# Optimization experiments

Hardware: AMD Instinct MI355X
Metric: run time of the kernel (lower is better)

## Reference

```python
import jax, jax.numpy as jnp
import numpy as np

M, IN, OUT = 8192, 4096, 4096
BITWIDTH = 7


def psto_shift_int32(x, shift):
    """Pseudo-stochastic right-shift of int32 x by `shift` bits -> int8.
    Faithful to PstoShiftInt32: floor-divide, derive a pseudo random number
    from the low half of the remainder, compare against the high half."""
    pow_s = jnp.left_shift(jnp.int32(1), shift)
    rt = jnp.floor_divide(x, pow_s)
    prob = jnp.abs(x - rt * pow_s)
    half_pow = jnp.left_shift(jnp.int32(1), shift // 2)
    qp = jnp.floor_divide(prob, half_pow)
    prn = prob - qp * half_pow
    prn = jnp.where(shift % 2 == 1, prn * 2, prn)
    dec = jnp.where(qp <= prn, jnp.int32(0), jnp.int32(1)) * jnp.sign(x)
    return jnp.clip(rt + dec, -127, 127).astype(jnp.int8)


def range_bitwidth(x):
    # RangeEstimate: ceil(log2(max|x|)), 0 if all-zero (torch also goes via float)
    m = jnp.max(jnp.abs(x)).astype(jnp.float32)
    return jnp.where(m == 0, jnp.int32(0), jnp.ceil(jnp.log2(m)).astype(jnp.int32))


def act_calc(acc, exp_in):
    """Shift int32 accumulator back to int8 and track the block exponent."""
    bw = range_bitwidth(acc)
    shift = bw - BITWIDTH
    # shift>1 -> shift by `shift`; shift==1 -> shift by 2; else -> plain int8 cast
    eff = jnp.where(shift > 1, shift, jnp.where(shift == 1, jnp.int32(2), jnp.int32(0)))
    rounded = psto_shift_int32(acc, jnp.maximum(eff, 0))
    out = jnp.where(eff > 0, rounded, acc.astype(jnp.int8))  # int8 cast wraps, as in torch
    exp_out = (exp_in + eff).astype(jnp.int8)
    return out, exp_out


def setup_inputs() -> dict:
    key = jax.random.key(0)
    k1, k2 = jax.random.split(key)
    # int8-valued tensors kept in int32 containers for the matmul accumulate
    act_in = jax.random.randint(k1, (M, IN), -127, 128, dtype=jnp.int32)
    weight = jax.random.randint(k2, (OUT, IN), -127, 128, dtype=jnp.int32)
    return {"act_in": act_in, "exp_in": -6, "weight": weight, "weight_exp": -9}


def reference(act_in, exp_in, weight, weight_exp):
    # the roundoff4 padding in the original is a no-op)
    acc = jnp.matmul(act_in, weight.T)  # [M, OUT] int32
    act_out, exp_out = act_calc(acc, jnp.int32(exp_in) + jnp.int32(weight_exp))
    return act_out, exp_out
```

## Files before the change

kernel.cpp:

```cpp
#include <hip/hip_runtime.h>
#include <stdint.h>
#include <math.h>

#define M_DIM 8192
#define N_DIM 4096
#define K_DIM 4096
#define BITWIDTH 7

#define BM 256
#define BN 128
#define BK 128
#define NT (K_DIM / BK)

using i32x4  = __attribute__((ext_vector_type(4)))  int;
using i32x16 = __attribute__((ext_vector_type(16))) int;

#define FENCE asm volatile("" ::: "memory")

__global__ __launch_bounds__(256) void pack_both_kernel(
        const int* __restrict__ act, const int* __restrict__ wt,
        uint32_t* __restrict__ a8p, uint32_t* __restrict__ w8,
        int* __restrict__ maxabs) {
    if (blockIdx.x == 0 && threadIdx.x == 0) *maxabs = 0;

    if (blockIdx.x < 8192) {
        const int tid = blockIdx.x * 256 + threadIdx.x;
        const int L  = tid & 63;
        const int kb = (tid >> 6) & 127;
        const int mb = tid >> 13;
        const size_t src = (size_t)(mb * 32 + (L & 31)) * K_DIM
                         + kb * 32 + (L >> 5) * 16;
        const int4* s = (const int4*)(act + src);
        uint32_t w[4];
#pragma unroll
        for (int q = 0; q < 4; ++q) {
            int4 v = s[q];
            w[q] = (uint32_t)(v.x & 0xFF) | ((uint32_t)(v.y & 0xFF) << 8)
                 | ((uint32_t)(v.z & 0xFF) << 16) | ((uint32_t)(v.w & 0xFF) << 24);
        }
        ((uint4*)a8p)[tid] = make_uint4(w[0], w[1], w[2], w[3]);
    } else {
        const int i = (blockIdx.x - 8192) * 256 + threadIdx.x;
        int4 a = ((const int4*)wt)[2 * i];
        int4 b = ((const int4*)wt)[2 * i + 1];
        uint32_t p0 = (uint32_t)(a.x & 0xFF) | ((uint32_t)(a.y & 0xFF) << 8)
                    | ((uint32_t)(a.z & 0xFF) << 16) | ((uint32_t)(a.w & 0xFF) << 24);
        uint32_t p1 = (uint32_t)(b.x & 0xFF) | ((uint32_t)(b.y & 0xFF) << 8)
                    | ((uint32_t)(b.z & 0xFF) << 16) | ((uint32_t)(b.w & 0xFF) << 24);
        ((uint2*)w8)[i] = make_uint2(p0, p1);
    }
}

__device__ __forceinline__ void gload_lds16(const int8_t* g, int8_t* lds) {
    __builtin_amdgcn_global_load_lds(
        (__attribute__((address_space(1))) void*)g,
        (__attribute__((address_space(3))) void*)lds,
        16, 0, 0);
}

__device__ __forceinline__ void load_af(i32x4 (&d)[2], const int8_t* aBase,
                                        int tkk) {
#pragma unroll
    for (int i = 0; i < 2; ++i)
        d[i] = *(const i32x4*)(aBase + (size_t)((i * 128 + tkk) << 10));
}

__device__ __forceinline__ void load_bf(i32x4 (&d)[4], const int8_t* bbuf,
                                        const int (&ro)[4], int co) {
#pragma unroll
    for (int j = 0; j < 4; ++j)
        d[j] = *(const i32x4*)(bbuf + ro[j] + co);
}

__device__ __forceinline__ void kkstep(const i32x4 (&a)[2], const i32x4 (&b)[4],
                                       i32x16 (&acc)[2][4]) {
#pragma unroll
    for (int i = 0; i < 2; ++i)
#pragma unroll
        for (int j = 0; j < 4; ++j)
            acc[i][j] = __builtin_amdgcn_mfma_i32_32x32x32_i8(
                a[i], b[j], acc[i][j], 0, 0, 0);
}

__global__ __launch_bounds__(256, 2) void gemm_i8(
        const int8_t* __restrict__ A8p, const int8_t* __restrict__ B8,
        int* __restrict__ C, int* __restrict__ maxabs) {
    __shared__ __align__(16) int8_t Bs[2][BN * BK];
    __shared__ int wmaxs[4];
    int8_t* BsF = &Bs[0][0];

    const int tid  = threadIdx.x;
    const int wave = tid >> 6;
    const int lane = tid & 63;
    const int fr   = lane & 31;
    const int hl   = lane >> 5;

    const int row0 = blockIdx.y * BM;
    const int col0 = blockIdx.x * BN;

    const int wm = wave * 64;

    i32x16 acc[2][4];
#pragma unroll
    for (int i = 0; i < 2; ++i)
#pragma unroll
        for (int j = 0; j < 4; ++j)
            acc[i][j] = (i32x16)(0);

    const int srowoff = lane >> 3;
    const int schk    = ((lane & 7) ^ srowoff) << 4;
    const int8_t* bg  = B8 + (size_t)(col0 + wave * 8 + srowoff) * K_DIM + schk;
    const int ldsoB   = wave * 1024;

    const int mbase = (row0 >> 5) + wave * 2;
    const int8_t* aBase = A8p + ((size_t)mbase << 17) + (size_t)lane * 16;

    const int swz = fr & 7;
    int rowOff[4];
#pragma unroll
    for (int j = 0; j < 4; ++j)
        rowOff[j] = (j * 32 + fr) * BK;
    int co[4];
#pragma unroll
    for (int kk = 0; kk < 4; ++kk)
        co[kk] = ((kk * 2 + hl) ^ swz) << 4;

    i32x4 afE[2], afO[2], bfE[4], bfO[4];

#pragma unroll
    for (int g = 0; g < 4; ++g)
        gload_lds16(bg + (size_t)(32 * g) * K_DIM, BsF + ldsoB + g * 4096);
    FENCE;
    load_af(afE, aBase, 0);
    asm volatile("s_waitcnt vmcnt(2)" ::: "memory");
    __builtin_amdgcn_s_barrier();

    for (int t = 0; t < NT - 1; ++t) {
        const int8_t* bbuf = BsF + ((t & 1) << 14);
        int8_t* bstg = BsF + (((t + 1) & 1) << 14) + ldsoB;
        const int kg = (t + 1) * BK;

        load_bf(bfE, bbuf, rowOff, co[0]); FENCE;
        load_af(afO, aBase, t * 4 + 1);    FENCE;
#pragma unroll
        for (int g = 0; g < 4; ++g)
            gload_lds16(bg + kg + (size_t)(32 * g) * K_DIM, bstg + g * 4096);
        FENCE;
        load_bf(bfO, bbuf, rowOff, co[1]); FENCE;
        kkstep(afE, bfE, acc);
        load_af(afE, aBase, t * 4 + 2);
        load_bf(bfE, bbuf, rowOff, co[2]); FENCE;
        kkstep(afO, bfO, acc);
        load_af(afO, aBase, t * 4 + 3);
        load_bf(bfO, bbuf, rowOff, co[3]); FENCE;
        kkstep(afE, bfE, acc);
        load_af(afE, aBase, t * 4 + 4);    FENCE;
        kkstep(afO, bfO, acc);
        asm volatile("s_waitcnt vmcnt(2)" ::: "memory");
        __builtin_amdgcn_s_barrier();
    }

    {
        const int tl = NT - 1;
        const int8_t* bbuf = BsF + ((tl & 1) << 14);
        load_bf(bfE, bbuf, rowOff, co[0]);
        load_af(afO, aBase, tl * 4 + 1);
        load_bf(bfO, bbuf, rowOff, co[1]); FENCE;
        kkstep(afE, bfE, acc);
        load_af(afE, aBase, tl * 4 + 2);
        load_bf(bfE, bbuf, rowOff, co[2]); FENCE;
        kkstep(afO, bfO, acc);
        load_af(afO, aBase, tl * 4 + 3);
        load_bf(bfO, bbuf, rowOff, co[3]); FENCE;
        kkstep(afE, bfE, acc);
        kkstep(afO, bfO, acc);
    }

    int mymax = 0;
    const int ccol = fr;
    const int rbase = hl << 2;
#pragma unroll
    for (int i = 0; i < 2; ++i) {
#pragma unroll
        for (int j = 0; j < 4; ++j) {
            int* p = C + (size_t)(row0 + wm + i * 32) * N_DIM
                       + (col0 + j * 32 + ccol);
#pragma unroll
            for (int r = 0; r < 16; ++r) {
                int row = (r & 3) + 8 * (r >> 2) + rbase;
                int v = acc[i][j][r];
                p[(size_t)row * N_DIM] = v;
                int a = v < 0 ? -v : v;
                mymax = a > mymax ? a : mymax;
            }
        }
    }

#pragma unroll
    for (int off = 32; off > 0; off >>= 1) {
        int o = __shfl_down(mymax, off, 64);
        mymax = o > mymax ? o : mymax;
    }
    if (lane == 0) wmaxs[wave] = mymax;
    __syncthreads();
    if (tid == 0) {
        int bmx = wmaxs[0];
        for (int w = 1; w < 4; ++w) bmx = wmaxs[w] > bmx ? wmaxs[w] : bmx;
        atomicMax(maxabs, bmx);
    }
}

__device__ __forceinline__ int psto(int x, int eff) {
    if (eff > 0) {
        int rt   = x >> eff;
        int prob = x & ((1 << eff) - 1);
        int h    = eff >> 1;
        int qp   = prob >> h;
        int prn  = (prob & ((1 << h) - 1)) << (eff & 1);
        int sgn  = (x > 0) - (x < 0);
        int r    = rt + ((qp <= prn) ? 0 : sgn);
        r = r < -127 ? -127 : r;
        r = r > 127 ? 127 : r;
        return r;
    }
    return (int)(int8_t)x;
}

__global__ __launch_bounds__(256) void finalize_kernel(int* __restrict__ C,
        const int* __restrict__ maxabs,
        const int* __restrict__ exp_in,
        const int* __restrict__ wexp) {
    const int m = *maxabs;
    int bw = 0;
    if (m != 0) bw = (int)ceilf(log2f((float)m));
    const int shift = bw - BITWIDTH;
    const int eff = (shift > 1) ? shift : ((shift == 1) ? 2 : 0);

    const size_t idx = ((size_t)blockIdx.x * blockDim.x + threadIdx.x) * 8;
    int4 v0 = *(const int4*)(C + idx);
    int4 v1 = *(const int4*)(C + idx + 4);
    int4 o0, o1;
    o0.x = psto(v0.x, eff); o0.y = psto(v0.y, eff);
    o0.z = psto(v0.z, eff); o0.w = psto(v0.w, eff);
    o1.x = psto(v1.x, eff); o1.y = psto(v1.y, eff);
    o1.z = psto(v1.z, eff); o1.w = psto(v1.w, eff);
    *(int4*)(C + idx) = o0;
    *(int4*)(C + idx + 4) = o1;

    if (idx == 0) {
        C[(size_t)M_DIM * N_DIM] = (int)(int8_t)(exp_in[0] + wexp[0] + eff);
    }
}

extern "C" void kernel_launch(void* const* d_in, const int* in_sizes, int n_in,
                              void* d_out, int out_size, void* d_ws, size_t ws_size,
                              hipStream_t stream) {
    const int* act    = (const int*)d_in[0];
    const int* exp_in = (const int*)d_in[1];
    const int* wt     = (const int*)d_in[2];
    const int* wexp   = (const int*)d_in[3];

    int8_t* a8p    = (int8_t*)d_ws;
    int8_t* w8     = a8p + (size_t)M_DIM * K_DIM;
    int*    maxabs = (int*)(w8 + (size_t)N_DIM * K_DIM);

    pack_both_kernel<<<16384, 256, 0, stream>>>(
        act, wt, (uint32_t*)a8p, (uint32_t*)w8, maxabs);

    int* C = (int*)d_out;
    dim3 grid(N_DIM / BN, M_DIM / BM);
    gemm_i8<<<grid, 256, 0, stream>>>(a8p, w8, C, maxabs);

    finalize_kernel<<<((size_t)M_DIM * N_DIM / 8) / 256, 256, 0, stream>>>(
        C, maxabs, exp_in, wexp);
}
```

Measured before the change: 434.2 us.

## Restructure GEMM main loop into barrier-gated MFMA phases with setprio

Reworks the int8 GEMM inner loop so each of the four k-substeps loads B fragments into a single register set and then waits on LDS. Workgroup barriers bracket each MFMA block, and s_setprio raises wave priority during the MFMAs to ping-pong waves between load and compute phases. The peeled final iteration is folded into the loop under a predicate, and fewer B-fragment registers are needed. The cost is many more barriers and full lgkmcnt waits, which give up the previous register double-buffering overlap of LDS reads with MFMA.

```diff
diff --git a/kernel.cpp b/kernel.cpp
--- a/kernel.cpp
+++ b/kernel.cpp
@@ -125,7 +125,7 @@
     for (int kk = 0; kk < 4; ++kk)
         co[kk] = ((kk * 2 + hl) ^ swz) << 4;
 
-    i32x4 afE[2], afO[2], bfE[4], bfO[4];
+    i32x4 afE[2], afO[2], bfP[4];
 
 #pragma unroll
     for (int g = 0; g < 4; ++g)
@@ -135,45 +135,54 @@
     asm volatile("s_waitcnt vmcnt(2)" ::: "memory");
     __builtin_amdgcn_s_barrier();
 
-    for (int t = 0; t < NT - 1; ++t) {
+    for (int t = 0; t < NT; ++t) {
         const int8_t* bbuf = BsF + ((t & 1) << 14);
         int8_t* bstg = BsF + (((t + 1) & 1) << 14) + ldsoB;
+        const bool st = (t < NT - 1);
         const int kg = (t + 1) * BK;
 
-        load_bf(bfE, bbuf, rowOff, co[0]); FENCE;
+        load_bf(bfP, bbuf, rowOff, co[0]); FENCE;
         load_af(afO, aBase, t * 4 + 1);    FENCE;
-#pragma unroll
-        for (int g = 0; g < 4; ++g)
-            gload_lds16(bg + kg + (size_t)(32 * g) * K_DIM, bstg + g * 4096);
+        if (st) {
+#pragma unroll
+            for (int g = 0; g < 4; ++g)
+                gload_lds16(bg + kg + (size_t)(32 * g) * K_DIM, bstg + g * 4096);
+        }
         FENCE;
-        load_bf(bfO, bbuf, rowOff, co[1]); FENCE;
-        kkstep(afE, bfE, acc);
-        load_af(afE, aBase, t * 4 + 2);
-        load_bf(bfE, bbuf, rowOff, co[2]); FENCE;
-        kkstep(afO, bfO, acc);
-        load_af(afO, aBase, t * 4 + 3);
-        load_bf(bfO, bbuf, rowOff, co[3]); FENCE;
-        kkstep(afE, bfE, acc);
-        load_af(afE, aBase, t * 4 + 4);    FENCE;
-        kkstep(afO, bfO, acc);
+        __builtin_amdgcn_s_barrier();
+        asm volatile("s_waitcnt lgkmcnt(0)" ::: "memory");
+        __builtin_amdgcn_s_setprio(1);
+        kkstep(afE, bfP, acc);
+        __builtin_amdgcn_s_setprio(0);
+        __builtin_amdgcn_s_barrier();
+
+        load_bf(bfP, bbuf, rowOff, co[1]); FENCE;
+        load_af(afE, aBase, t * 4 + 2);    FENCE;
+        __builtin_amdgcn_s_barrier();
+        asm volatile("s_waitcnt lgkmcnt(0)" ::: "memory");
+        __builtin_amdgcn_s_setprio(1);
+        kkstep(afO, bfP, acc);
+        __builtin_amdgcn_s_setprio(0);
+        __builtin_amdgcn_s_barrier();
+
+        load_bf(bfP, bbuf, rowOff, co[2]); FENCE;
+        load_af(afO, aBase, t * 4 + 3);    FENCE;
+        __builtin_amdgcn_s_barrier();
+        asm volatile("s_waitcnt lgkmcnt(0)" ::: "memory");
+        __builtin_amdgcn_s_setprio(1);
+        kkstep(afE, bfP, acc);
+        __builtin_amdgcn_s_setprio(0);
+        __builtin_amdgcn_s_barrier();
+
+        load_bf(bfP, bbuf, rowOff, co[3]); FENCE;
+        load_af(afE, aBase, st ? (t * 4 + 4) : 0); FENCE;
+        __builtin_amdgcn_s_barrier();
+        asm volatile("s_waitcnt lgkmcnt(0)" ::: "memory");
+        __builtin_amdgcn_s_setprio(1);
+        kkstep(afO, bfP, acc);
+        __builtin_amdgcn_s_setprio(0);
         asm volatile("s_waitcnt vmcnt(2)" ::: "memory");
         __builtin_amdgcn_s_barrier();
-    }
-
-    {
-        const int tl = NT - 1;
-        const int8_t* bbuf = BsF + ((tl & 1) << 14);
-        load_bf(bfE, bbuf, rowOff, co[0]);
-        load_af(afO, aBase, tl * 4 + 1);
-        load_bf(bfO, bbuf, rowOff, co[1]); FENCE;
-        kkstep(afE, bfE, acc);
-        load_af(afE, aBase, tl * 4 + 2);
-        load_bf(bfE, bbuf, rowOff, co[2]); FENCE;
-        kkstep(afO, bfO, acc);
-        load_af(afO, aBase, tl * 4 + 3);
-        load_bf(bfO, bbuf, rowOff, co[3]); FENCE;
-        kkstep(afE, bfE, acc);
-        kkstep(afO, bfO, acc);
     }
 
     int mymax = 0;
```

After: 435.6 us. Within noise of the previous version (+0.3%).
